# Kernel optimization log

Hardware: AMD Instinct MI355X
Metric: run time of the kernel (lower is better)

## Reference

```python
import jax, jax.numpy as jnp
import numpy as np

NUM_HEADS = 16
HEAD_DIM = 64
BATCH = 4
SEQ = 1024
MAX_SEQ_LEN = 2048


def _shift(pos_score):
    # Transformer-XL relative shift. pos_score: (NH, S, S_kv)
    NH, S, S_kv = pos_score.shape
    zero_pad = jnp.zeros((NH, S, 1), dtype=pos_score.dtype)
    padded = jnp.concatenate([zero_pad, pos_score], axis=-1)  # (NH, S, S_kv+1)
    padded = padded.reshape(NH, S_kv + 1, S)
    return padded[:, 1:, :].reshape(NH, S, S_kv)


def setup_inputs() -> dict:
    key = jax.random.key(0)
    ks = jax.random.split(key, 6)
    NH = BATCH * NUM_HEADS
    return {
        "queries": jax.random.normal(ks[0], (NH, SEQ, HEAD_DIM), dtype=jnp.float32),
        "keys": jax.random.normal(ks[1], (NH, SEQ, HEAD_DIM), dtype=jnp.float32),
        "values": jax.random.normal(ks[2], (NH, SEQ, HEAD_DIM), dtype=jnp.float32),
        "u_bias": jax.random.normal(ks[3], (1, NUM_HEADS, 1, HEAD_DIM), dtype=jnp.float32),
        "v_bias": jax.random.normal(ks[4], (1, NUM_HEADS, 1, HEAD_DIM), dtype=jnp.float32),
        "R": jax.random.normal(ks[5], (NUM_HEADS, MAX_SEQ_LEN, HEAD_DIM), dtype=jnp.float32),
    }


def reference(queries, keys, values, u_bias, v_bias, R):
    NH, S, d = queries.shape
    S_kv = keys.shape[1]
    batch = NH // NUM_HEADS

    q = queries * (d ** -0.5)
    q = q.reshape(batch, NUM_HEADS, S, d)
    q_u = (q + u_bias).reshape(NH, S, d)
    q_v = (q + v_bias).reshape(NH, S, d)

    # relative position embeddings, tiled over batch: (NH, S_kv, d)
    R_s = jnp.tile(R[:, :S_kv, :], (batch, 1, 1))

    content_score = jnp.einsum('nsd,ntd->nst', q_u, keys)   # (NH, S, S_kv)
    pos_score = jnp.einsum('nsd,ntd->nst', q_v, R_s)        # (NH, S, S_kv)
    pos_score = _shift(pos_score)

    attn_weights = jax.nn.softmax(content_score + pos_score, axis=-1)
    attn = jnp.einsum('nst,ntd->nsd', attn_weights, values)  # (NH, S, d)
    return attn
```

## Files before the change

kernel.cpp:

```cpp
#include <hip/hip_runtime.h>


#define SQ    1024
#define HD    64
#define NHD   16
#define RMAX  2048

typedef _Float16 f16x8 __attribute__((ext_vector_type(8)));
typedef _Float16 f16x4 __attribute__((ext_vector_type(4)));
typedef _Float16 f16x2 __attribute__((ext_vector_type(2)));
typedef short    b16x8 __attribute__((ext_vector_type(8)));
typedef short    b16x4 __attribute__((ext_vector_type(4)));
typedef float    f32x4 __attribute__((ext_vector_type(4)));
typedef unsigned u32x2 __attribute__((ext_vector_type(2)));
typedef unsigned u32x4 __attribute__((ext_vector_type(4)));

#define MFMA_F16(A,B,C)  __builtin_amdgcn_mfma_f32_16x16x32_f16((A),(B),(C),0,0,0)
#define MFMA_BF16(A,B,C) __builtin_amdgcn_mfma_f32_16x16x32_bf16((A),(B),(C),0,0,0)

#define L2E    1.44269504088896f
#define NSHIFT (-57.7078016f)

#define KH_OFF   0
#define VT_OFF   (8u << 20)
#define R16_OFF  (18u << 20)
#define WS_NEED  (20u << 20)

__device__ __forceinline__ float exp2fast(float x) {
#if __has_builtin(__builtin_amdgcn_exp2f)
  return __builtin_amdgcn_exp2f(x);
#else
  return __expf(x * 0.693147180559945f);
#endif
}

__device__ __forceinline__ f32x4 mfma16bf(b16x4 a, b16x4 b, f32x4 c) {
#if __has_builtin(__builtin_amdgcn_mfma_f32_16x16x16bf16_1k)
  return __builtin_amdgcn_mfma_f32_16x16x16bf16_1k(a, b, c, 0, 0, 0);
#else
  b16x8 az = {a[0], a[1], a[2], a[3], 0, 0, 0, 0};
  b16x8 bz = {b[0], b[1], b[2], b[3], 0, 0, 0, 0};
  return MFMA_BF16(az, bz, c);
#endif
}

__device__ __forceinline__ short f2b(float f) {
  unsigned u = __builtin_bit_cast(unsigned, f);
  u += 0x7FFFu + ((u >> 16) & 1u);
  return (short)(u >> 16);
}
__device__ __forceinline__ unsigned pkh(float a, float b) {
#if __has_builtin(__builtin_amdgcn_cvt_pkrtz)
  return __builtin_bit_cast(unsigned, __builtin_amdgcn_cvt_pkrtz(a, b));
#else
  _Float16 h0 = (_Float16)a, h1 = (_Float16)b;
  return (unsigned)__builtin_bit_cast(unsigned short, h0)
       | ((unsigned)__builtin_bit_cast(unsigned short, h1) << 16);
#endif
}
__device__ __forceinline__ unsigned pkb2(float a, float b) {
  unsigned ua = __builtin_bit_cast(unsigned, a) + 0x8000u;
  unsigned ub = __builtin_bit_cast(unsigned, b) + 0x8000u;
  return (ub & 0xFFFF0000u) | (ua >> 16);
}
__device__ __forceinline__ float h2f(unsigned w, int sh) {
  return (float)__builtin_bit_cast(_Float16, (unsigned short)(w >> sh));
}
__device__ __forceinline__ int swz(int row, int col) {
  return row*64 + ((((col >> 3) ^ row) & 7) << 3) + (col & 7);
}
__device__ __forceinline__ int swzv(int row, int col) {
  return row*64 + ((((col >> 3) ^ row) & 7) << 3)
       + ((col & 7) ^ ((row & 8) >> 1));
}


__global__ __launch_bounds__(256) void preprep(
    const float* __restrict__ K, const float* __restrict__ R,
    const float* __restrict__ V,
    _Float16* __restrict__ Kh, _Float16* __restrict__ R16,
    short* __restrict__ Vt)
{
  __shared__ float t[64][65];
  const int bid = blockIdx.x, tid = threadIdx.x;
  if (bid < 1024) {
    const int n = bid >> 4, st = bid & 15;
    {
      const int row = tid >> 2, c0 = (tid & 3) * 16;
      const float* src = V + ((size_t)n * SQ + st * 64 + row) * HD + c0;
#pragma unroll
      for (int i = 0; i < 4; ++i) {
        float4 x = ((const float4*)src)[i];
        t[row][c0 + 4*i + 0] = x.x; t[row][c0 + 4*i + 1] = x.y;
        t[row][c0 + 4*i + 2] = x.z; t[row][c0 + 4*i + 3] = x.w;
      }
    }
    __syncthreads();
    {
      const int d = tid >> 2, s0 = (tid & 3) * 16;
      const int xo = (d & 8) ? 4 : 0;
      short* dst = Vt + ((size_t)n * 80 + d) * SQ + st * 64 + s0;
#pragma unroll
      for (int i = 0; i < 8; ++i)
        *(unsigned*)(dst + (2*i ^ xo)) = pkb2(t[s0 + 2*i][d], t[s0 + 2*i + 1][d]);
    }
    if (tid < 64) {
      const int s = st * 64 + tid;
      Vt[((size_t)n * 80 + 64) * SQ + s] = (short)0x3F80;
#pragma unroll
      for (int r = 65; r < 80; ++r) Vt[((size_t)n * 80 + r) * SQ + s] = 0;
    }
  } else {
    const int idx = (bid - 1024) * 256 + tid;
    const int nk4 = (64 * SQ * HD) / 4;
    if (idx < nk4) {
      float4 v = ((const float4*)K)[idx];
      f16x4 o = { (_Float16)v.x, (_Float16)v.y, (_Float16)v.z, (_Float16)v.w };
      *(f16x4*)(Kh + 4 * (size_t)idx) = o;
    } else {
      int rr = idx - nk4;
      int h  = rr >> 14, off = rr & 16383;
      float4 v = ((const float4*)R)[((size_t)h << 15) + off];
      f16x4 o = { (_Float16)v.x, (_Float16)v.y, (_Float16)v.z, (_Float16)v.w };
      *(f16x4*)(R16 + 4 * (((size_t)h << 14) + off)) = o;
    }
  }
}


__global__ __launch_bounds__(256, 3) void relpos_sdpa_r18(
    const float* __restrict__ Q, const _Float16* __restrict__ Kh,
    const short* __restrict__ Vtg, const _Float16* __restrict__ R16,
    const float* __restrict__ Ub, const float* __restrict__ Vb,
    float* __restrict__ O)
{
  const int n    = blockIdx.x;
  const int h    = n & (NHD - 1);
  const int a0   = blockIdx.y * 64;
  const int tid  = threadIdx.x;
  const int lane = tid & 63, wave = tid >> 6;
  const int l15  = lane & 15, quad = lane >> 4;

  const float*    Qn  = Q   + (size_t)n * SQ * HD;
  const _Float16* Khn = Kh  + (size_t)n * SQ * HD;
  const short*    Vgn = Vtg + (size_t)n * 80 * SQ;
  const _Float16* Rh  = R16 + (size_t)h * SQ * HD;

  __shared__ __align__(16) char lds[50192];
  unsigned*       Pb2  = (unsigned*)(lds + 32768);
  const _Float16* Pb2h = (const _Float16*)Pb2;

  auto gload16 = [&](const void* g, void* l) {
#if __has_builtin(__builtin_amdgcn_global_load_lds)
    __builtin_amdgcn_global_load_lds(
        (const __attribute__((address_space(1))) unsigned*)g,
        (__attribute__((address_space(3))) unsigned*)l, 16, 0, 0);
#else
    *(u32x4*)((char*)l + lane * 16) = *(const u32x4*)g;
#endif
  };
  auto dmaStage = [&](int kk, int buf) {
    const int rb = lane >> 3;
    const int g  = (lane & 7) ^ ((lane >> 3) & 7);
    char* kdst = lds + buf * 8192;
    char* vdst = lds + 16384 + buf * 8192;
#pragma unroll
    for (int i = 0; i < 2; ++i) {
      const int sub = 2*wave + i;
      const int r   = 8*sub + rb;
      gload16(Khn + (size_t)(kk + r) * HD + 8*g, kdst + sub * 1024);
      gload16(Vgn + (size_t)r * SQ + kk + 8*g,   vdst + sub * 1024);
    }
  };

  dmaStage(0, 0);

  f16x8 quF[2], qvF[5][2];
#pragma unroll
  for (int ks = 0; ks < 2; ++ks) {
    const int db = ks * 32 + quad * 8;
    float ub[8], vb[8];
#pragma unroll
    for (int j = 0; j < 8; ++j) {
      ub[j] = Ub[h*HD + db + j] * L2E;
      vb[j] = Vb[h*HD + db + j] * L2E;
    }
    {
      const float* p = Qn + (size_t)(a0 + 16*wave + l15) * HD + db;
      float4 x0 = ((const float4*)p)[0], x1 = ((const float4*)p)[1];
      f16x8 f;
#pragma unroll
      for (int t = 0; t < 4; ++t) {
        f[t]   = (_Float16)((&x0.x)[t] * (0.125f * L2E) + ub[t]);
        f[t+4] = (_Float16)((&x1.x)[t] * (0.125f * L2E) + ub[t+4]);
      }
      quF[ks] = f;
    }
#pragma unroll
    for (int rt = 0; rt < 5; ++rt) {
      int row = a0 + 16*rt + l15; if (row > SQ-1) row = SQ-1;
      const float* p = Qn + (size_t)row * HD + db;
      float4 x0 = ((const float4*)p)[0], x1 = ((const float4*)p)[1];
      f16x8 f;
#pragma unroll
      for (int t = 0; t < 4; ++t) {
        f[t]   = (_Float16)((&x0.x)[t] * (0.125f * L2E) + vb[t]);
        f[t+4] = (_Float16)((&x1.x)[t] * (0.125f * L2E) + vb[t+4]);
      }
      qvF[rt][ks] = f;
    }
  }

  f32x4 Oacc[4], acc_l;
#pragma unroll
  for (int ct = 0; ct < 4; ++ct) Oacc[ct] = (f32x4){0.f, 0.f, 0.f, 0.f};
  acc_l = (f32x4){0.f, 0.f, 0.f, 0.f};

  const b16x4 ONESB = {(short)0x3F80, (short)0x3F80, (short)0x3F80, (short)0x3F80};

  unsigned ringW[9];
  int ringSlot, ringSlotN;
  f16x8 bB0, bB1;
  auto bandLoad = [&](int jstart) {
    const int c = jstart + 16*wave + l15;
    const int j = (c + 2048) & (SQ - 1);
    ringSlotN   = (c + 2048) & 127;
    const _Float16* rp = Rh + (size_t)j * HD + quad * 8;
    bB0 = *(const f16x8*)rp;
    bB1 = *(const f16x8*)(rp + 32);
  };
  auto bandMFMA = [&]() {
    ringSlot = ringSlotN;
    __builtin_amdgcn_s_setprio(1);
#pragma unroll
    for (int rt = 0; rt < 5; ++rt) {
      f32x4 acc = (f32x4){0.f, 0.f, 0.f, 0.f};
      acc = MFMA_F16(qvF[rt][0], bB0, acc);
      acc = MFMA_F16(qvF[rt][1], bB1, acc);
      if (rt < 4) {
        ringW[2*rt]     = pkh(acc[0], acc[1]);
        ringW[2*rt + 1] = pkh(acc[2], acc[3]);
      } else {
        ringW[8] = pkh(acc[0], acc[1]);
      }
    }
    __builtin_amdgcn_s_setprio(0);
  };
  auto ringFlush = [&]() {
#pragma unroll
    for (int rt = 0; rt < 4; ++rt) {
      const int rp0 = 8*rt + 2*quad;
      Pb2[rp0*132 + ringSlot]       = ringW[2*rt];
      Pb2[(rp0 + 1)*132 + ringSlot] = ringW[2*rt + 1];
    }
    if (quad == 0) Pb2[32*132 + ringSlot] = ringW[8];
    if (ringSlot < 3) {
      const int ms = ringSlot + 128;
#pragma unroll
      for (int rt = 0; rt < 4; ++rt) {
        const int rp0 = 8*rt + 2*quad;
        Pb2[rp0*132 + ms]       = ringW[2*rt];
        Pb2[(rp0 + 1)*132 + ms] = ringW[2*rt + 1];
      }
      if (quad == 0) Pb2[32*132 + ms] = ringW[8];
    }
  };

  bandLoad(-a0 - 65);  bandMFMA();  ringFlush();
  bandLoad(-a0 - 1);   bandMFMA();  ringFlush();

  const int iiB = 16*wave + 4*quad;
  const int iQ  = 16*wave + l15;

  int cur = 0;
  for (int k0 = 0; k0 < SQ; k0 += 64) {
    __builtin_amdgcn_sched_barrier(0);
    asm volatile("s_waitcnt lgkmcnt(0)" ::: "memory");
    __builtin_amdgcn_s_barrier();
    __builtin_amdgcn_sched_barrier(0);

    if (k0 > 0) ringFlush();
    if (k0 < SQ - 64) {
      bandLoad(k0 + 64 - a0 - 1);
      dmaStage(k0 + 64, cur ^ 1);
      __builtin_amdgcn_sched_barrier(0);
      asm volatile("s_waitcnt vmcnt(6) lgkmcnt(0)" ::: "memory");
    } else {
      __builtin_amdgcn_sched_barrier(0);
      asm volatile("s_waitcnt vmcnt(0) lgkmcnt(0)" ::: "memory");
    }
    __builtin_amdgcn_s_barrier();
    __builtin_amdgcn_sched_barrier(0);

    const _Float16* Kb = (const _Float16*)(lds + (cur << 13));
    const short*    Vt = (const short*)(lds + 16384 + (cur << 13));

    const int  base  = k0 - a0 - 16*wave;
    const bool gFast = !(k0 == a0 || k0 == a0 + 64);
    unsigned gw[16];
    int shG = 0;
    if (gFast) {
      const int u  = (k0 > a0) ? 1 : 0;
      const int iu = iQ + u;
      const unsigned* wrow = &Pb2[(iu >> 1) * 132];
      shG = (iu & 1) << 4;
      const int sb = base - 1 - u + 4*quad - l15 + 2048;
#pragma unroll
      for (int ct = 0; ct < 4; ++ct) {
        const int s0 = (sb + 16*ct) & 127;
        gw[4*ct + 0] = wrow[s0];
        gw[4*ct + 1] = wrow[s0 + 1];
        gw[4*ct + 2] = wrow[s0 + 2];
        gw[4*ct + 3] = wrow[s0 + 3];
      }
    }

    f32x4 sc[4];
    __builtin_amdgcn_s_setprio(1);
#pragma unroll
    for (int ct = 0; ct < 4; ++ct) {
      f16x8 ka = *(const f16x8*)&Kb[swz(16*ct + l15, quad*8)];
      f16x8 kb = *(const f16x8*)&Kb[swz(16*ct + l15, 32 + quad*8)];
      f32x4 acc = (f32x4){NSHIFT, NSHIFT, NSHIFT, NSHIFT};
      acc = MFMA_F16(ka, quF[0], acc);
      acc = MFMA_F16(kb, quF[1], acc);
      sc[ct] = acc;
    }
    __builtin_amdgcn_s_setprio(0);

    if (gFast) {
#pragma unroll
      for (int ct = 0; ct < 4; ++ct) {
        sc[ct][0] = exp2fast(sc[ct][0] + h2f(gw[4*ct + 0], shG));
        sc[ct][1] = exp2fast(sc[ct][1] + h2f(gw[4*ct + 1], shG));
        sc[ct][2] = exp2fast(sc[ct][2] + h2f(gw[4*ct + 2], shG));
        sc[ct][3] = exp2fast(sc[ct][3] + h2f(gw[4*ct + 3], shG));
      }
    } else {
      const int adA = (iQ >> 1) * 264 + (iQ & 1);
      const int adB = ((iQ + 1) >> 1) * 264 + ((iQ + 1) & 1);
#pragma unroll
      for (int ct = 0; ct < 4; ++ct) {
        const int e0 = base + 16*ct + 4*quad - l15;
#pragma unroll
        for (int r = 0; r < 4; ++r) {
          const int e    = e0 + r;
          const int u    = (e > 0) ? 1 : 0;
          const int slot = (e - 1 - u) & 127;
          float pos = (float)Pb2h[(u ? adB : adA) + 2*slot];
          float s   = sc[ct][r] + ((e == 1) ? 0.f : pos);
          sc[ct][r] = exp2fast(s);
        }
      }
    }

    __builtin_amdgcn_s_setprio(1);
#pragma unroll
    for (int ctk = 0; ctk < 4; ++ctk) {
      unsigned lo = pkb2(sc[ctk][0], sc[ctk][1]);
      unsigned hi = pkb2(sc[ctk][2], sc[ctk][3]);
      b16x4 aF = __builtin_bit_cast(b16x4, (u32x2){lo, hi});
      acc_l = mfma16bf(aF, ONESB, acc_l);
#pragma unroll
      for (int ctd = 0; ctd < 4; ++ctd) {
        b16x4 bF = *(const b16x4*)&Vt[swzv(16*ctd + l15, 16*ctk + 4*quad)];
        Oacc[ctd] = mfma16bf(aF, bF, Oacc[ctd]);
      }
    }
    __builtin_amdgcn_s_setprio(0);

    if (k0 < SQ - 64) bandMFMA();
    cur ^= 1;
  }

#pragma unroll
  for (int r = 0; r < 4; ++r) {
    float inv = 1.0f / acc_l[r];
    const size_t rowo = (size_t)n * SQ * HD + (size_t)(a0 + iiB + r) * HD;
#pragma unroll
    for (int ct = 0; ct < 4; ++ct)
      O[rowo + 16*ct + l15] = Oacc[ct][r] * inv;
  }
}


__global__ __launch_bounds__(256, 4) void relpos_sdpa_fb(
    const float* __restrict__ Q, const float* __restrict__ K,
    const float* __restrict__ V, const float* __restrict__ Ub,
    const float* __restrict__ Vb, const float* __restrict__ R,
    float* __restrict__ O)
{
  const int n    = blockIdx.x;
  const int h    = n & (NHD - 1);
  const int a0   = blockIdx.y * 64;
  const int tid  = threadIdx.x;
  const int lane = tid & 63, wave = tid >> 6;
  const int l15  = lane & 15, quad = lane >> 4;

  const float* Qn = Q + (size_t)n * SQ * HD;
  const float* Kn = K + (size_t)n * SQ * HD;
  const float* Vn = V + (size_t)n * SQ * HD;
  const float* Rh = R + (size_t)h * RMAX * HD;

  __shared__ __align__(16) char lds[38656];
  _Float16* Kb = (_Float16*)lds;
  short*    Ps = (short*)lds;
  short*    Vt = (short*)(lds + 9216);
  _Float16* Pb = (_Float16*)(lds + 9216 + 11520);

  f16x8 quF[2], qvF[5][2];
#pragma unroll
  for (int ks = 0; ks < 2; ++ks) {
    const int db = ks * 32 + quad * 8;
    float ub[8], vb[8];
#pragma unroll
    for (int j = 0; j < 8; ++j) { ub[j] = Ub[h*HD + db + j]; vb[j] = Vb[h*HD + db + j]; }
    {
      const float* p = Qn + (size_t)(a0 + 16*wave + l15) * HD + db;
      f16x8 f;
#pragma unroll
      for (int j = 0; j < 8; ++j) f[j] = (_Float16)(p[j] * 0.125f + ub[j]);
      quF[ks] = f;
    }
#pragma unroll
    for (int rt = 0; rt < 5; ++rt) {
      int row = a0 + 16*rt + l15; if (row > SQ-1) row = SQ-1;
      const float* p = Qn + (size_t)row * HD + db;
      f16x8 f;
#pragma unroll
      for (int j = 0; j < 8; ++j) f[j] = (_Float16)(p[j] * 0.125f + vb[j]);
      qvF[rt][ks] = f;
    }
  }

  if (tid < 64) Vt[64*72 + tid] = (short)0x3F80;

  f32x4 Oacc[5];
#pragma unroll
  for (int ct = 0; ct < 5; ++ct) Oacc[ct] = (f32x4){0.f, 0.f, 0.f, 0.f};

  auto band = [&](int jstart) {
    const int c    = jstart + 16*wave + l15;
    const int j    = (c + 2048) & (SQ - 1);
    const int slot = (c + 2048) & 127;
    const float* rp = Rh + (size_t)j * HD + quad * 8;
    f16x8 B0, B1;
    {
      float4 x0 = *(const float4*)(rp),      x1 = *(const float4*)(rp + 4);
      float4 y0 = *(const float4*)(rp + 32), y1 = *(const float4*)(rp + 36);
#pragma unroll
      for (int t = 0; t < 4; ++t) { B0[t] = (_Float16)(&x0.x)[t]; B0[t+4] = (_Float16)(&x1.x)[t]; }
#pragma unroll
      for (int t = 0; t < 4; ++t) { B1[t] = (_Float16)(&y0.x)[t]; B1[t+4] = (_Float16)(&y1.x)[t]; }
    }
#pragma unroll
    for (int rt = 0; rt < 5; ++rt) {
      f32x4 acc = (f32x4){0.f, 0.f, 0.f, 0.f};
      acc = MFMA_F16(qvF[rt][0], B0, acc);
      acc = MFMA_F16(qvF[rt][1], B1, acc);
      const int row = 16*rt + 4*quad;
      if (rt < 4) {
        *(unsigned*)&Pb[slot*70 + row]     = pkh(acc[0], acc[1]);
        *(unsigned*)&Pb[slot*70 + row + 2] = pkh(acc[2], acc[3]);
      } else if (quad == 0) {
        *(unsigned*)&Pb[slot*70 + row]     = pkh(acc[0], acc[1]);
      }
    }
  };

  band(-a0 - 65);
  band(-a0 - 1);

  const int sr = tid >> 2, sc4 = tid & 3;
  const int iiB = 16*wave + 4*quad;

  for (int k0 = 0; k0 < SQ; k0 += 64) {
    __syncthreads();
    {
      const float* src = Kn + (size_t)(k0 + sr) * HD + sc4 * 16;
      float4 x0 = *(const float4*)(src),     x1 = *(const float4*)(src + 4);
      float4 y0 = *(const float4*)(src + 8), y1 = *(const float4*)(src + 12);
      f16x8 lo, hi;
#pragma unroll
      for (int t = 0; t < 4; ++t) { lo[t] = (_Float16)(&x0.x)[t]; lo[t+4] = (_Float16)(&x1.x)[t]; }
#pragma unroll
      for (int t = 0; t < 4; ++t) { hi[t] = (_Float16)(&y0.x)[t]; hi[t+4] = (_Float16)(&y1.x)[t]; }
      *(f16x8*)&Kb[sr*72 + sc4*16]     = lo;
      *(f16x8*)&Kb[sr*72 + sc4*16 + 8] = hi;
    }
    {
      const int g = lane >> 3;
#pragma unroll
      for (int i = 0; i < 8; ++i) {
        int bp = 8*wave + (i ^ g);
        float v0 = Vn[(size_t)(k0 + 2*bp)     * HD + lane];
        float v1 = Vn[(size_t)(k0 + 2*bp + 1) * HD + lane];
        *(unsigned*)&Vt[lane*72 + 2*bp] = pkb2(v0, v1);
      }
    }
    __syncthreads();

    f32x4 sc[4];
#pragma unroll
    for (int ct = 0; ct < 4; ++ct) {
      f16x8 b0 = *(const f16x8*)&Kb[(16*ct + l15)*72 + quad*8];
      f16x8 b1 = *(const f16x8*)&Kb[(16*ct + l15)*72 + 32 + quad*8];
      f32x4 acc = (f32x4){0.f, 0.f, 0.f, 0.f};
      acc = MFMA_F16(quF[0], b0, acc);
      acc = MFMA_F16(quF[1], b1, acc);
      sc[ct] = acc;
    }

    const int dlt = k0 - a0;
#pragma unroll
    for (int r = 0; r < 4; ++r) {
      const int ii = iiB + r;
#pragma unroll
      for (int ct = 0; ct < 4; ++ct) {
        const int e    = dlt + 16*ct + l15 - ii;
        const int u    = (e > 0) ? 1 : 0;
        const int slot = (e - 1 - u + 2048) & 127;
        float pos = (float)Pb[slot*70 + ii + u];
        float s   = sc[ct][r] + ((e == 1) ? 0.f : pos);
        sc[ct][r] = __expf(s - 40.0f);
      }
    }
    __syncthreads();

#pragma unroll
    for (int r = 0; r < 4; ++r)
#pragma unroll
      for (int ct = 0; ct < 4; ++ct)
        Ps[(iiB + r)*68 + 16*ct + l15] = f2b(sc[ct][r]);

    b16x8 pA0 = *(const b16x8*)&Ps[(16*wave + l15)*68 + quad*8];
    b16x8 pA1 = *(const b16x8*)&Ps[(16*wave + l15)*68 + 32 + quad*8];
#pragma unroll
    for (int ct = 0; ct < 5; ++ct) {
      b16x8 v0 = *(const b16x8*)&Vt[(16*ct + l15)*72 + quad*8];
      b16x8 v1 = *(const b16x8*)&Vt[(16*ct + l15)*72 + 32 + quad*8];
      Oacc[ct] = MFMA_BF16(pA0, v0, Oacc[ct]);
      Oacc[ct] = MFMA_BF16(pA1, v1, Oacc[ct]);
    }

    if (k0 < SQ - 64) band(k0 + 64 - a0 - 1);
  }

#pragma unroll
  for (int r = 0; r < 4; ++r) {
    float l   = __shfl(Oacc[4][r], lane & 48);
    float inv = 1.0f / l;
    const size_t rowo = (size_t)n * SQ * HD + (size_t)(a0 + iiB + r) * HD;
#pragma unroll
    for (int ct = 0; ct < 4; ++ct)
      O[rowo + 16*ct + l15] = Oacc[ct][r] * inv;
  }
}

extern "C" void kernel_launch(void* const* d_in, const int* in_sizes, int n_in,
                              void* d_out, int out_size, void* d_ws, size_t ws_size,
                              hipStream_t stream) {
  const float* Q  = (const float*)d_in[0];
  const float* K  = (const float*)d_in[1];
  const float* V  = (const float*)d_in[2];
  const float* Ub = (const float*)d_in[3];
  const float* Vb = (const float*)d_in[4];
  const float* R  = (const float*)d_in[5];
  float* O = (float*)d_out;

  if (ws_size >= WS_NEED) {
    _Float16* Kh  = (_Float16*)((char*)d_ws + KH_OFF);
    short*    Vt  = (short*)((char*)d_ws + VT_OFF);
    _Float16* R16 = (_Float16*)((char*)d_ws + R16_OFF);

    preprep<<<6144, 256, 0, stream>>>(K, R, V, Kh, R16, Vt);

    dim3 grid(64, 16);
    relpos_sdpa_r18<<<grid, 256, 0, stream>>>(Q, Kh, Vt, R16, Ub, Vb, O);
  } else {
    dim3 grid(64, 16);
    relpos_sdpa_fb<<<grid, 256, 0, stream>>>(Q, K, V, Ub, Vb, R, O);
  }
}
```

Before: 165.9 us.

## Load K fragments straight into registers with double buffering, dropping K LDS staging

K tiles are no longer staged through LDS. Each lane now loads its MFMA K fragments directly from global memory into two register sets that alternate, and the loop is unrolled by two to swap them. This frees 16KB of LDS and removes the K LDS reads, and the QK MFMAs are issued before the wait on the V DMA. In exchange register pressure rises, launch bounds drop from 3 to 2 waves per SIMD, and every wave now reads K from global memory redundantly.

```diff
diff --git a/kernel.cpp b/kernel.cpp
--- a/kernel.cpp
+++ b/kernel.cpp
@@ -8,7 +8,6 @@
 
 typedef _Float16 f16x8 __attribute__((ext_vector_type(8)));
 typedef _Float16 f16x4 __attribute__((ext_vector_type(4)));
-typedef _Float16 f16x2 __attribute__((ext_vector_type(2)));
 typedef short    b16x8 __attribute__((ext_vector_type(8)));
 typedef short    b16x4 __attribute__((ext_vector_type(4)));
 typedef float    f32x4 __attribute__((ext_vector_type(4)));
@@ -50,13 +49,9 @@
   return (short)(u >> 16);
 }
 __device__ __forceinline__ unsigned pkh(float a, float b) {
-#if __has_builtin(__builtin_amdgcn_cvt_pkrtz)
-  return __builtin_bit_cast(unsigned, __builtin_amdgcn_cvt_pkrtz(a, b));
-#else
   _Float16 h0 = (_Float16)a, h1 = (_Float16)b;
   return (unsigned)__builtin_bit_cast(unsigned short, h0)
        | ((unsigned)__builtin_bit_cast(unsigned short, h1) << 16);
-#endif
 }
 __device__ __forceinline__ unsigned pkb2(float a, float b) {
   unsigned ua = __builtin_bit_cast(unsigned, a) + 0x8000u;
@@ -65,9 +60,6 @@
 }
 __device__ __forceinline__ float h2f(unsigned w, int sh) {
   return (float)__builtin_bit_cast(_Float16, (unsigned short)(w >> sh));
-}
-__device__ __forceinline__ int swz(int row, int col) {
-  return row*64 + ((((col >> 3) ^ row) & 7) << 3) + (col & 7);
 }
 __device__ __forceinline__ int swzv(int row, int col) {
   return row*64 + ((((col >> 3) ^ row) & 7) << 3)
@@ -128,7 +120,7 @@
 }
 
 
-__global__ __launch_bounds__(256, 3) void relpos_sdpa_r18(
+__global__ __launch_bounds__(256, 2) void relpos_sdpa_r19(
     const float* __restrict__ Q, const _Float16* __restrict__ Kh,
     const short* __restrict__ Vtg, const _Float16* __restrict__ R16,
     const float* __restrict__ Ub, const float* __restrict__ Vb,
@@ -146,8 +138,8 @@
   const short*    Vgn = Vtg + (size_t)n * 80 * SQ;
   const _Float16* Rh  = R16 + (size_t)h * SQ * HD;
 
-  __shared__ __align__(16) char lds[50192];
-  unsigned*       Pb2  = (unsigned*)(lds + 32768);
+  __shared__ __align__(16) char lds[33808];
+  unsigned*       Pb2  = (unsigned*)(lds + 16384);
   const _Float16* Pb2h = (const _Float16*)Pb2;
 
   auto gload16 = [&](const void* g, void* l) {
@@ -159,21 +151,30 @@
     *(u32x4*)((char*)l + lane * 16) = *(const u32x4*)g;
 #endif
   };
-  auto dmaStage = [&](int kk, int buf) {
+  auto dmaStageV = [&](int kk, int buf) {
     const int rb = lane >> 3;
     const int g  = (lane & 7) ^ ((lane >> 3) & 7);
-    char* kdst = lds + buf * 8192;
-    char* vdst = lds + 16384 + buf * 8192;
+    char* vdst = lds + buf * 8192;
 #pragma unroll
     for (int i = 0; i < 2; ++i) {
       const int sub = 2*wave + i;
       const int r   = 8*sub + rb;
-      gload16(Khn + (size_t)(kk + r) * HD + 8*g, kdst + sub * 1024);
-      gload16(Vgn + (size_t)r * SQ + kk + 8*g,   vdst + sub * 1024);
-    }
-  };
-
-  dmaStage(0, 0);
+      gload16(Vgn + (size_t)r * SQ + kk + 8*g, vdst + sub * 1024);
+    }
+  };
+
+  f16x8 kfA[4][2], kfB[4][2];
+  auto kLoad = [&](int kk, f16x8 (&kF)[4][2]) {
+#pragma unroll
+    for (int ct = 0; ct < 4; ++ct) {
+      const _Float16* kp = Khn + (size_t)(kk + 16*ct + l15) * HD + quad*8;
+      kF[ct][0] = *(const f16x8*)kp;
+      kF[ct][1] = *(const f16x8*)(kp + 32);
+    }
+  };
+
+  dmaStageV(0, 0);
+  kLoad(0, kfA);
 
   f16x8 quF[2], qvF[5][2];
 #pragma unroll
@@ -272,28 +273,38 @@
   const int iiB = 16*wave + 4*quad;
   const int iQ  = 16*wave + l15;
 
-  int cur = 0;
-  for (int k0 = 0; k0 < SQ; k0 += 64) {
+  auto iterBody = [&](int k0, f16x8 (&kU)[4][2], f16x8 (&kN)[4][2], int buf) {
     __builtin_amdgcn_sched_barrier(0);
     asm volatile("s_waitcnt lgkmcnt(0)" ::: "memory");
     __builtin_amdgcn_s_barrier();
     __builtin_amdgcn_sched_barrier(0);
 
     if (k0 > 0) ringFlush();
-    if (k0 < SQ - 64) {
+    const bool notLast = (k0 < SQ - 64);
+    if (notLast) {
       bandLoad(k0 + 64 - a0 - 1);
-      dmaStage(k0 + 64, cur ^ 1);
-      __builtin_amdgcn_sched_barrier(0);
-      asm volatile("s_waitcnt vmcnt(6) lgkmcnt(0)" ::: "memory");
-    } else {
-      __builtin_amdgcn_sched_barrier(0);
-      asm volatile("s_waitcnt vmcnt(0) lgkmcnt(0)" ::: "memory");
-    }
+      kLoad(k0 + 64, kN);
+      dmaStageV(k0 + 64, buf ^ 1);
+    }
+
+    f32x4 sc[4];
+    __builtin_amdgcn_s_setprio(1);
+#pragma unroll
+    for (int ct = 0; ct < 4; ++ct) {
+      f32x4 acc = (f32x4){NSHIFT, NSHIFT, NSHIFT, NSHIFT};
+      acc = MFMA_F16(kU[ct][0], quF[0], acc);
+      acc = MFMA_F16(kU[ct][1], quF[1], acc);
+      sc[ct] = acc;
+    }
+    __builtin_amdgcn_s_setprio(0);
+
+    __builtin_amdgcn_sched_barrier(0);
+    if (notLast) asm volatile("s_waitcnt vmcnt(12) lgkmcnt(0)" ::: "memory");
+    else         asm volatile("s_waitcnt vmcnt(0) lgkmcnt(0)" ::: "memory");
     __builtin_amdgcn_s_barrier();
     __builtin_amdgcn_sched_barrier(0);
 
-    const _Float16* Kb = (const _Float16*)(lds + (cur << 13));
-    const short*    Vt = (const short*)(lds + 16384 + (cur << 13));
+    const short* Vt = (const short*)(lds + (buf << 13));
 
     const int  base  = k0 - a0 - 16*wave;
     const bool gFast = !(k0 == a0 || k0 == a0 + 64);
@@ -315,19 +326,6 @@
       }
     }
 
-    f32x4 sc[4];
-    __builtin_amdgcn_s_setprio(1);
-#pragma unroll
-    for (int ct = 0; ct < 4; ++ct) {
-      f16x8 ka = *(const f16x8*)&Kb[swz(16*ct + l15, quad*8)];
-      f16x8 kb = *(const f16x8*)&Kb[swz(16*ct + l15, 32 + quad*8)];
-      f32x4 acc = (f32x4){NSHIFT, NSHIFT, NSHIFT, NSHIFT};
-      acc = MFMA_F16(ka, quF[0], acc);
-      acc = MFMA_F16(kb, quF[1], acc);
-      sc[ct] = acc;
-    }
-    __builtin_amdgcn_s_setprio(0);
-
     if (gFast) {
 #pragma unroll
       for (int ct = 0; ct < 4; ++ct) {
@@ -369,8 +367,12 @@
     }
     __builtin_amdgcn_s_setprio(0);
 
-    if (k0 < SQ - 64) bandMFMA();
-    cur ^= 1;
+    if (notLast) bandMFMA();
+  };
+
+  for (int k0 = 0; k0 < SQ; k0 += 128) {
+    iterBody(k0,      kfA, kfB, 0);
+    iterBody(k0 + 64, kfB, kfA, 1);
   }
 
 #pragma unroll
@@ -576,7 +578,7 @@
     preprep<<<6144, 256, 0, stream>>>(K, R, V, Kh, R16, Vt);
 
     dim3 grid(64, 16);
-    relpos_sdpa_r18<<<grid, 256, 0, stream>>>(Q, Kh, Vt, R16, Ub, Vb, O);
+    relpos_sdpa_r19<<<grid, 256, 0, stream>>>(Q, Kh, Vt, R16, Ub, Vb, O);
   } else {
     dim3 grid(64, 16);
     relpos_sdpa_fb<<<grid, 256, 0, stream>>>(Q, K, V, Ub, Vb, R, O);
```

Result: slower. 193.0 us (+16.3%).
